# Kernel optimization log

Measured on AMD Instinct MI355X. Metric: run time of the kernel, lower is better.

The kernel has to match this reference:

```python
import jax, jax.numpy as jnp
import numpy as np

N_NODES = 50000
ALPHA_SLOPE = 0.2  # LeakyReLU negative slope
EPS = 1e-16


def setup_inputs() -> dict:
    key = jax.random.key(0)
    k1, k2, k3, k4 = jax.random.split(key, 4)
    in_features, heads, d = 512, 8, 32
    x = jax.random.normal(k1, (N_NODES, in_features), dtype=jnp.float32)
    edge_index = jax.random.randint(k2, (2, 800000), 0, N_NODES, dtype=jnp.int64)
    # xavier_normal with relu gain ~ sqrt(2) * sqrt(2/(fan_in+fan_out))
    w_std = np.sqrt(2.0) * np.sqrt(2.0 / (in_features + d))
    a_std = np.sqrt(2.0) * np.sqrt(2.0 / (1 + 2 * d))
    W = jax.random.normal(k3, (heads, in_features, d), dtype=jnp.float32) * w_std
    a = jax.random.normal(k4, (heads, 2 * d), dtype=jnp.float32) * a_std
    return {"x": x, "edge_index": edge_index, "W": W, "a": a}


def reference(x, edge_index, W, a):
    # x: [N, F_in], edge_index: [2, E], W: [H, F_in, D], a: [H, 2D]
    n = x.shape[0]
    d = W.shape[-1]
    e0, e1 = edge_index[0], edge_index[1]
    # per-head projected features: [N, H, D]
    h = jnp.einsum('nf,hfd->nhd', x, W)
    # attention logits: a.mm(cat(h[e0], h[e1]).T) == a_src.h[e0] + a_dst.h[e1]
    a_src, a_dst = a[:, :d], a[:, d:]          # [H, D] each
    s_src = jnp.einsum('nhd,hd->nh', h, a_src)  # [N, H]
    s_dst = jnp.einsum('nhd,hd->nh', h, a_dst)  # [N, H]
    logits = s_src[e0] + s_dst[e1]              # [E, H]
    logits = jnp.where(logits >= 0, logits, ALPHA_SLOPE * logits)  # LeakyReLU
    # segment softmax over destination node e0
    m = jax.ops.segment_max(logits, e0, num_segments=n)   # [N, H]
    ex = jnp.exp(logits - m[e0])                          # [E, H]
    denom = jax.ops.segment_sum(ex, e0, num_segments=n)   # [N, H]
    alpha = ex / (denom[e0] + EPS)                        # [E, H]
    # dropout is identity in eval mode
    # sparse aggregate: out[e0] += alpha * h[e1]
    msg = alpha[:, :, None] * h[e1]                       # [E, H, D]
    out = jax.ops.segment_sum(msg, e0, num_segments=n)    # [N, H, D]
    return out.reshape(n, -1)                             # concat heads -> [N, H*D]
```

## Files before the change

### kernel.cpp

```cpp
#include <hip/hip_runtime.h>

#define N_NODES 50000
#define N_EDGES 800000
#define IN_F    512
#define HEADS   8
#define DHEAD   32
#define NHD     256
#define SLOPE   0.2f
#define EPS_F   1e-16f
#define N_SBLK  ((N_NODES + 255) / 256)
#define NB_GEMM ((N_NODES + 63) / 64)
#define NB_HIST ((N_EDGES + 4095) / 4096)

typedef __attribute__((ext_vector_type(8))) short short8;
typedef __attribute__((ext_vector_type(4))) float f32x4;
typedef __attribute__((ext_vector_type(4))) unsigned short u16x4;

__device__ __forceinline__ unsigned short f2bf(float f) {
  unsigned int u = __float_as_uint(f);
  unsigned int r = u + 0x7FFFu + ((u >> 16) & 1u);
  return (unsigned short)(r >> 16);
}
__device__ __forceinline__ float bf2f(unsigned short s) {
  return __uint_as_float(((unsigned int)s) << 16);
}

__global__ __launch_bounds__(256) void k_cast_w(const float* __restrict__ W,
                                                unsigned short* __restrict__ WbT,
                                                int* __restrict__ deg) {
  int id = blockIdx.x * 256 + threadIdx.x;
  int chunk = id >> 3, e = id & 7;
  int lane = chunk & 63;
  int t = chunk >> 6;
  int j = t & 7;  t >>= 3;
  int wn2 = t & 1; t >>= 1;
  int kk = t & 1;  t >>= 1;
  int k0s = t;
  int c = wn2 * 128 + j * 16 + (lane & 15);
  int k = k0s * 64 + (kk * 4 + (lane >> 4)) * 8 + e;
  WbT[id] = f2bf(W[(c >> 5) * (IN_F * DHEAD) + k * DHEAD + (c & 31)]);
  if (id < N_NODES) deg[id] = 0;
}

__global__ __launch_bounds__(256) void k_gemm_mfma(const float* __restrict__ x,
                                                   const unsigned short* __restrict__ WbT,
                                                   unsigned short* __restrict__ hb,
                                                   const float* __restrict__ a,
                                                   float* __restrict__ s_src,
                                                   float* __restrict__ s_dst,
                                                   const int* __restrict__ ei,
                                                   int* __restrict__ deg) {
  if (blockIdx.x >= NB_GEMM) {
    int b = blockIdx.x - NB_GEMM;
    int end = min(b * 4096 + 4096, N_EDGES);
    for (int e = b * 4096 + threadIdx.x; e < end; e += 256)
      atomicAdd(&deg[ei[e]], 1);
    return;
  }

  const int tid  = threadIdx.x;
  const int lane = tid & 63;
  const int wid  = tid >> 6;
  const int wm   = wid >> 1;
  const int wn2  = wid & 1;
  const int bm   = blockIdx.x * 64;
  const int dl   = lane & 15;
  const int qg   = lane >> 4;

  const float* xr[2];
#pragma unroll
  for (int i = 0; i < 2; ++i)
    xr[i] = x + (size_t)min(bm + wm * 32 + i * 16 + dl, N_NODES - 1) * IN_F + qg * 8;

  f32x4 acc[2][8] = {};

#pragma unroll 2
  for (int k0s = 0; k0s < 8; ++k0s) {
#pragma unroll
    for (int kk = 0; kk < 2; ++kk) {
      const unsigned short* bp =
          WbT + (((size_t)((k0s * 2 + kk) * 2 + wn2) * 8) * 64 + lane) * 8;
      short8 bfr[8];
#pragma unroll
      for (int j = 0; j < 8; ++j) bfr[j] = *(const short8*)(bp + (size_t)j * 64 * 8);
      short8 af[2];
#pragma unroll
      for (int i = 0; i < 2; ++i) {
        const float* ap = xr[i] + k0s * 64 + kk * 32;
        float4 lo = *(const float4*)ap;
        float4 hi = *(const float4*)(ap + 4);
        short8 v;
        v[0] = (short)f2bf(lo.x); v[1] = (short)f2bf(lo.y);
        v[2] = (short)f2bf(lo.z); v[3] = (short)f2bf(lo.w);
        v[4] = (short)f2bf(hi.x); v[5] = (short)f2bf(hi.y);
        v[6] = (short)f2bf(hi.z); v[7] = (short)f2bf(hi.w);
        af[i] = v;
      }
#pragma unroll
      for (int i = 0; i < 2; ++i)
#pragma unroll
        for (int j = 0; j < 8; ++j)
          acc[i][j] = __builtin_amdgcn_mfma_f32_16x16x32_bf16(af[i], bfr[j], acc[i][j], 0, 0, 0);
    }
  }

  float as_[8], ad_[8];
#pragma unroll
  for (int j = 0; j < 8; ++j) {
    int hh = wn2 * 4 + (j >> 1);
    int d  = (j & 1) * 16 + dl;
    as_[j] = a[hh * 64 + d];
    ad_[j] = a[hh * 64 + 32 + d];
  }
#pragma unroll
  for (int i = 0; i < 2; ++i) {
#pragma unroll
    for (int q = 0; q < 4; ++q) {
      int row = bm + wm * 32 + i * 16 + qg * 4 + q;
      float ss[4] = {0.f, 0.f, 0.f, 0.f};
      float sd[4] = {0.f, 0.f, 0.f, 0.f};
#pragma unroll
      for (int j = 0; j < 8; ++j) {
        ss[j >> 1] += acc[i][j][q] * as_[j];
        sd[j >> 1] += acc[i][j][q] * ad_[j];
      }
#pragma unroll
      for (int o = 1; o < 16; o <<= 1) {
#pragma unroll
        for (int h2 = 0; h2 < 4; ++h2) {
          ss[h2] += __shfl_xor(ss[h2], o);
          sd[h2] += __shfl_xor(sd[h2], o);
        }
      }
      if (row < N_NODES) {
#pragma unroll
        for (int j = 0; j < 8; ++j)
          hb[(size_t)row * NHD + wn2 * 128 + j * 16 + dl] = f2bf(acc[i][j][q]);
        if (dl == 0) {
#pragma unroll
          for (int h2 = 0; h2 < 4; ++h2) {
            s_src[row * 8 + wn2 * 4 + h2] = ss[h2];
            s_dst[row * 8 + wn2 * 4 + h2] = sd[h2];
          }
        }
      }
    }
  }
}

__global__ __launch_bounds__(256) void k_bsum(const int* __restrict__ deg,
                                              int* __restrict__ bsum) {
  __shared__ int sm[4];
  int i = blockIdx.x * 256 + threadIdx.x;
  int v = (i < N_NODES) ? deg[i] : 0;
#pragma unroll
  for (int o = 1; o < 64; o <<= 1) v += __shfl_xor(v, o);
  if ((threadIdx.x & 63) == 0) sm[threadIdx.x >> 6] = v;
  __syncthreads();
  if (threadIdx.x == 0) bsum[blockIdx.x] = sm[0] + sm[1] + sm[2] + sm[3];
}

__global__ __launch_bounds__(256) void k_scan_main(const int* __restrict__ deg,
                                                   const int* __restrict__ bsum,
                                                   int* __restrict__ rowptr,
                                                   int* __restrict__ cursor) {
  __shared__ int sb[256];
  __shared__ int sm[256];
  const int t = threadIdx.x;
  const int b = blockIdx.x;
  int bv = (t < N_SBLK) ? bsum[t] : 0;
  sb[t] = bv;
  int i = b * 256 + t;
  int v = (i < N_NODES) ? deg[i] : 0;
  sm[t] = v;
  __syncthreads();
#pragma unroll
  for (int o = 1; o < 256; o <<= 1) {
    int u1 = (t >= o) ? sb[t - o] : 0;
    int u2 = (t >= o) ? sm[t - o] : 0;
    __syncthreads();
    sb[t] += u1;
    sm[t] += u2;
    __syncthreads();
  }
  int boff = (b > 0) ? sb[b - 1] : 0;
  if (i < N_NODES) {
    int ex = boff + sm[t] - v;
    rowptr[i] = ex;
    cursor[i] = ex;
  }
  if (b == 0 && t == 0) rowptr[N_NODES] = sb[255];
}

__global__ void k_fill(const int* __restrict__ ei, int* __restrict__ cursor,
                       int* __restrict__ edst) {
  int e = blockIdx.x * blockDim.x + threadIdx.x;
  if (e >= N_EDGES) return;
  int p = atomicAdd(&cursor[ei[e]], 1);
  edst[p] = ei[N_EDGES + e];
}

__global__ __launch_bounds__(256) void k_aggr(const int* __restrict__ rowptr,
                                              const int* __restrict__ edst,
                                              const float* __restrict__ s_src,
                                              const float* __restrict__ s_dst,
                                              const unsigned short* __restrict__ hb,
                                              float* __restrict__ out) {
  int n = (int)((blockIdx.x * blockDim.x + threadIdx.x) >> 6);
  if (n >= N_NODES) return;
  n = __builtin_amdgcn_readfirstlane(n);
  const int lane = threadIdx.x & 63;
  const int head = lane >> 3;
  const float ssrc = s_src[n * 8 + head];
  int i = rowptr[n];
  const int iend = rowptr[n + 1];
  float den = 0.f;
  f32x4 acc = {0.f, 0.f, 0.f, 0.f};
  for (; i + 1 < iend; i += 2) {
    int d0 = edst[i], d1 = edst[i + 1];
    float v0 = ssrc + s_dst[d0 * 8 + head];
    float v1 = ssrc + s_dst[d1 * 8 + head];
    u16x4 h0 = *(const u16x4*)(hb + (size_t)d0 * NHD + lane * 4);
    u16x4 h1 = *(const u16x4*)(hb + (size_t)d1 * NHD + lane * 4);
    v0 = v0 >= 0.f ? v0 : SLOPE * v0;
    v1 = v1 >= 0.f ? v1 : SLOPE * v1;
    float e0 = __expf(v0), e1 = __expf(v1);
    den += e0 + e1;
    acc.x += e0 * bf2f(h0.x) + e1 * bf2f(h1.x);
    acc.y += e0 * bf2f(h0.y) + e1 * bf2f(h1.y);
    acc.z += e0 * bf2f(h0.z) + e1 * bf2f(h1.z);
    acc.w += e0 * bf2f(h0.w) + e1 * bf2f(h1.w);
  }
  if (i < iend) {
    int d0 = edst[i];
    float v0 = ssrc + s_dst[d0 * 8 + head];
    v0 = v0 >= 0.f ? v0 : SLOPE * v0;
    float e0 = __expf(v0);
    u16x4 h0 = *(const u16x4*)(hb + (size_t)d0 * NHD + lane * 4);
    den += e0;
    acc.x += e0 * bf2f(h0.x);
    acc.y += e0 * bf2f(h0.y);
    acc.z += e0 * bf2f(h0.z);
    acc.w += e0 * bf2f(h0.w);
  }
  float inv = 1.f / (den + EPS_F);
  *(f32x4*)(out + (size_t)n * NHD + lane * 4) = acc * inv;
}

extern "C" void kernel_launch(void* const* d_in, const int* in_sizes, int n_in,
                              void* d_out, int out_size, void* d_ws, size_t ws_size,
                              hipStream_t stream) {
  const float* x  = (const float*)d_in[0];
  const int*   ei = (const int*)d_in[1];
  const float* W  = (const float*)d_in[2];
  const float* a  = (const float*)d_in[3];
  float* out = (float*)d_out;

  unsigned short* hb  = (unsigned short*)d_ws;
  unsigned short* WbT = hb + (size_t)N_NODES * NHD;
  float* s_src = (float*)(WbT + (size_t)NHD * IN_F);
  float* s_dst = s_src + (size_t)N_NODES * HEADS;
  int* deg    = (int*)(s_dst + (size_t)N_NODES * HEADS);
  int* cursor = deg + N_NODES;
  int* rowptr = cursor + N_NODES;
  int* bsum   = rowptr + 50008;
  int* edst   = bsum + 256;

  k_cast_w<<<512, 256, 0, stream>>>(W, WbT, deg);
  k_gemm_mfma<<<NB_GEMM + NB_HIST, 256, 0, stream>>>(x, WbT, hb, a, s_src, s_dst, ei, deg);
  k_bsum<<<N_SBLK, 256, 0, stream>>>(deg, bsum);
  k_scan_main<<<N_SBLK, 256, 0, stream>>>(deg, bsum, rowptr, cursor);
  k_fill<<<(N_EDGES + 255) / 256, 256, 0, stream>>>(ei, cursor, edst);
  k_aggr<<<(N_NODES * 64 + 255) / 256, 256, 0, stream>>>(rowptr, edst, s_src, s_dst, hb, out);
}
```

Baseline: 194.2 us.

## Stage GEMM tiles in LDS with swizzled layout and 128-row blocks

Rewrites the projection GEMM so each block loads a 128x64 bf16 tile of x and the full 256x64 W tile into shared memory per k-step. W is copied with direct global-to-LDS loads, and XOR swizzling is meant to avoid bank conflicts. Each wave now computes 64 rows instead of 32, which increases operand reuse and cuts redundant global reads of W. W is stored in plain row-major [c][k] bf16 and converted with packed bf16 intrinsics. The cost is higher register pressure from 32 accumulators, a large LDS footprint that lowers occupancy, and two barriers per k-step.

```diff
diff --git a/kernel.cpp b/kernel.cpp
--- a/kernel.cpp
+++ b/kernel.cpp
@@ -1,4 +1,5 @@
 #include <hip/hip_runtime.h>
+#include <hip/hip_bf16.h>
 
 #define N_NODES 50000
 #define N_EDGES 800000
@@ -9,12 +10,13 @@
 #define SLOPE   0.2f
 #define EPS_F   1e-16f
 #define N_SBLK  ((N_NODES + 255) / 256)
-#define NB_GEMM ((N_NODES + 63) / 64)
+#define NB_GEMM ((N_NODES + 127) / 128)
 #define NB_HIST ((N_EDGES + 4095) / 4096)
 
 typedef __attribute__((ext_vector_type(8))) short short8;
 typedef __attribute__((ext_vector_type(4))) float f32x4;
 typedef __attribute__((ext_vector_type(4))) unsigned short u16x4;
+typedef __attribute__((ext_vector_type(4))) unsigned int u32x4;
 
 __device__ __forceinline__ unsigned short f2bf(float f) {
   unsigned int u = __float_as_uint(f);
@@ -24,21 +26,24 @@
 __device__ __forceinline__ float bf2f(unsigned short s) {
   return __uint_as_float(((unsigned int)s) << 16);
 }
-
-__global__ __launch_bounds__(256) void k_cast_w(const float* __restrict__ W,
-                                                unsigned short* __restrict__ WbT,
-                                                int* __restrict__ deg) {
-  int id = blockIdx.x * 256 + threadIdx.x;
-  int chunk = id >> 3, e = id & 7;
-  int lane = chunk & 63;
-  int t = chunk >> 6;
-  int j = t & 7;  t >>= 3;
-  int wn2 = t & 1; t >>= 1;
-  int kk = t & 1;  t >>= 1;
-  int k0s = t;
-  int c = wn2 * 128 + j * 16 + (lane & 15);
-  int k = k0s * 64 + (kk * 4 + (lane >> 4)) * 8 + e;
-  WbT[id] = f2bf(W[(c >> 5) * (IN_F * DHEAD) + k * DHEAD + (c & 31)]);
+__device__ __forceinline__ unsigned int pkbf(float a, float b) {
+  __hip_bfloat162 t = __float22bfloat162_rn(float2{a, b});
+  unsigned int r;
+  __builtin_memcpy(&r, &t, sizeof(r));
+  return r;
+}
+__device__ __forceinline__ void gload_lds16(const void* g, void* l) {
+  __builtin_amdgcn_global_load_lds((const __attribute__((address_space(1))) void*)g,
+                                   (__attribute__((address_space(3))) void*)l, 16, 0, 0);
+}
+
+__global__ void k_cast_w(const float* __restrict__ W, unsigned short* __restrict__ WbT,
+                         int* __restrict__ deg) {
+  int id = blockIdx.x * blockDim.x + threadIdx.x;
+  if (id < NHD * IN_F) {
+    int c = id >> 9, k = id & 511;
+    WbT[id] = f2bf(W[(c >> 5) * (IN_F * DHEAD) + k * DHEAD + (c & 31)]);
+  }
   if (id < N_NODES) deg[id] = 0;
 }
 
@@ -58,52 +63,73 @@
     return;
   }
 
+  __shared__ unsigned short As[128 * 64];
+  __shared__ unsigned short Bs[256 * 64];
   const int tid  = threadIdx.x;
   const int lane = tid & 63;
   const int wid  = tid >> 6;
   const int wm   = wid >> 1;
   const int wn2  = wid & 1;
-  const int bm   = blockIdx.x * 64;
-  const int dl   = lane & 15;
-  const int qg   = lane >> 4;
-
-  const float* xr[2];
-#pragma unroll
-  for (int i = 0; i < 2; ++i)
-    xr[i] = x + (size_t)min(bm + wm * 32 + i * 16 + dl, N_NODES - 1) * IN_F + qg * 8;
-
-  f32x4 acc[2][8] = {};
-
-#pragma unroll 2
-  for (int k0s = 0; k0s < 8; ++k0s) {
+  const int bm   = blockIdx.x * 128;
+
+  const int ar = tid >> 1, ahf = tid & 1;
+  const float* gA = x + (size_t)min(bm + ar, N_NODES - 1) * IN_F + ahf * 32;
+  unsigned short* lArow = &As[ar * 64];
+
+  const int bc0 = wid * 64 + (lane >> 3);
+  const int bgq = (lane & 7) ^ ((lane >> 3) & 7);
+  const unsigned short* gB0 = WbT + (size_t)bc0 * IN_F + bgq * 8;
+  unsigned short* lBw = &Bs[((size_t)wid * 64 * 8 + lane) * 8];
+
+  f32x4 acc[4][8] = {};
+
+#pragma unroll
+  for (int t = 0; t < 8; ++t) {
+    const int k0 = t * 64;
+    __syncthreads();
+#pragma unroll
+    for (int it = 0; it < 8; ++it)
+      gload_lds16(gB0 + k0 + it * 8 * IN_F, lBw + it * 64 * 8);
+    {
+      float4 f[8];
+#pragma unroll
+      for (int m = 0; m < 8; ++m) f[m] = ((const float4*)(gA + k0))[m];
+#pragma unroll
+      for (int m = 0; m < 4; ++m) {
+        u32x4 v = { pkbf(f[2 * m].x, f[2 * m].y),  pkbf(f[2 * m].z, f[2 * m].w),
+                    pkbf(f[2 * m + 1].x, f[2 * m + 1].y), pkbf(f[2 * m + 1].z, f[2 * m + 1].w) };
+        int p = (ahf * 4 + m) ^ (ar & 7);
+        *(u32x4*)&lArow[p * 8] = v;
+      }
+    }
+    __syncthreads();
+
+    const int dl = lane & 15;
+    const int qg = lane >> 4;
 #pragma unroll
     for (int kk = 0; kk < 2; ++kk) {
-      const unsigned short* bp =
-          WbT + (((size_t)((k0s * 2 + kk) * 2 + wn2) * 8) * 64 + lane) * 8;
-      short8 bfr[8];
-#pragma unroll
-      for (int j = 0; j < 8; ++j) bfr[j] = *(const short8*)(bp + (size_t)j * 64 * 8);
-      short8 af[2];
-#pragma unroll
-      for (int i = 0; i < 2; ++i) {
-        const float* ap = xr[i] + k0s * 64 + kk * 32;
-        float4 lo = *(const float4*)ap;
-        float4 hi = *(const float4*)(ap + 4);
-        short8 v;
-        v[0] = (short)f2bf(lo.x); v[1] = (short)f2bf(lo.y);
-        v[2] = (short)f2bf(lo.z); v[3] = (short)f2bf(lo.w);
-        v[4] = (short)f2bf(hi.x); v[5] = (short)f2bf(hi.y);
-        v[6] = (short)f2bf(hi.z); v[7] = (short)f2bf(hi.w);
-        af[i] = v;
-      }
-#pragma unroll
-      for (int i = 0; i < 2; ++i)
+      const int kq = kk * 4 + qg;
+      short8 af[4], bfr[8];
+#pragma unroll
+      for (int i = 0; i < 4; ++i) {
+        int r = wm * 64 + i * 16 + dl;
+        af[i] = *(const short8*)&As[(r * 8 + (kq ^ (r & 7))) * 8];
+      }
+#pragma unroll
+      for (int j = 0; j < 8; ++j) {
+        int c = wn2 * 128 + j * 16 + dl;
+        bfr[j] = *(const short8*)&Bs[(c * 8 + (kq ^ (c & 7))) * 8];
+      }
+#pragma unroll
+      for (int i = 0; i < 4; ++i)
 #pragma unroll
         for (int j = 0; j < 8; ++j)
           acc[i][j] = __builtin_amdgcn_mfma_f32_16x16x32_bf16(af[i], bfr[j], acc[i][j], 0, 0, 0);
     }
   }
 
+  const int dl = lane & 15;
+  const int qg = lane >> 4;
   float as_[8], ad_[8];
 #pragma unroll
   for (int j = 0; j < 8; ++j) {
@@ -113,10 +139,10 @@
     ad_[j] = a[hh * 64 + 32 + d];
   }
 #pragma unroll
-  for (int i = 0; i < 2; ++i) {
+  for (int i = 0; i < 4; ++i) {
 #pragma unroll
     for (int q = 0; q < 4; ++q) {
-      int row = bm + wm * 32 + i * 16 + qg * 4 + q;
+      int row = bm + wm * 64 + i * 16 + qg * 4 + q;
       float ss[4] = {0.f, 0.f, 0.f, 0.f};
       float sd[4] = {0.f, 0.f, 0.f, 0.f};
 #pragma unroll
```

Measured after the change: 195.2 us. About the same (+0.5%).
